# Performance work log

Measured on AMD Instinct MI355X. Metric: run time of the kernel, lower is better.

Reference implementation:

```python
import math
import jax, jax.numpy as jnp
import numpy as np

B, T, D = 2, 2048, 1024
NH = 16
HD = D // NH


def setup_inputs() -> dict:
    key = jax.random.key(0)
    k1, k2, k3 = jax.random.split(key, 3)
    s = 0.02
    return {
        "x": jax.random.normal(k1, (B, T, D), dtype=jnp.float32),
        "w_qkv": jax.random.normal(k2, (D, 3 * D), dtype=jnp.float32) * s,
        "w_proj": jax.random.normal(k3, (D, D), dtype=jnp.float32) * s,
    }


def reference(x, w_qkv, w_proj):
    b, t, c = x.shape
    qkv = x @ w_qkv  # [B,T,3D]
    q, k, v = jnp.split(qkv, 3, axis=-1)
    # [B,NH,T,HD]
    q = q.reshape(b, t, NH, HD).transpose(0, 2, 1, 3)
    k = k.reshape(b, t, NH, HD).transpose(0, 2, 1, 3)
    v = v.reshape(b, t, NH, HD).transpose(0, 2, 1, 3)
    scores = jnp.einsum("bhqd,bhkd->bhqk", q, k) / math.sqrt(HD)
    mask = jnp.tril(jnp.ones((t, t), dtype=x.dtype))  # [T,T]
    # faithful to source: scaled scores are multiplied by the mask, then -1e9 added where masked
    masked = scores * mask + (1.0 - mask) * (-1e9)
    a = jax.nn.softmax(masked, axis=-1)
    out = jnp.einsum("bhqk,bhkd->bhqd", a, v)  # [B,NH,T,HD]
    out = out.transpose(0, 2, 1, 3).reshape(b, t, c)
    return out @ w_proj
```

## Files before the change

kernel.cpp:

```cpp
#include <hip/hip_runtime.h>
#include <stdint.h>

#define B_SZ 2
#define T_SEQ 2048
#define D_MODEL 1024
#define NHEADS 16
#define HDIM 64
#define QKV_P (3 * D_MODEL)

typedef unsigned short u16;
typedef uint32_t u32;
typedef __attribute__((ext_vector_type(4))) float f32x4;
typedef __attribute__((ext_vector_type(8))) short s16x8;
typedef __attribute__((ext_vector_type(4))) short s16x4;

__device__ __forceinline__ u16 f2bf(float f) {
  union { float f; uint32_t u; } v; v.f = f;
  uint32_t r = v.u + 0x7fffu + ((v.u >> 16) & 1u);
  return (u16)(r >> 16);
}

__device__ __forceinline__ float fastexp2(float x) {
  float r;
  asm volatile("v_exp_f32 %0, %1" : "=v"(r) : "v"(x));
  return r;
}

__device__ __forceinline__ u32 cvtpk(float lo, float hi) {
  u32 r;
  asm volatile("v_cvt_pk_bf16_f32 %0, %1, %2" : "=v"(r) : "v"(lo), "v"(hi));
  return r;
}

__device__ __forceinline__ void async16(const void* g, void* l) {
  __builtin_amdgcn_global_load_lds((const __attribute__((address_space(1))) void*)g,
                                   (__attribute__((address_space(3))) void*)l,
                                   16, 0, 0);
}

__device__ __forceinline__ void rawbar() {
  __builtin_amdgcn_s_barrier();
  __builtin_amdgcn_sched_barrier(0);
}

__global__ __launch_bounds__(256) void prep(const float* __restrict__ x,
                                            const float* __restrict__ wq,
                                            const float* __restrict__ wp,
                                            u16* __restrict__ xb,
                                            u16* __restrict__ wqkvT,
                                            u16* __restrict__ wprojT) {
  const int bid = blockIdx.x, tid = threadIdx.x;
  if (bid < 4096) {
    int i = bid * 256 + tid;
    float4 v = ((const float4*)x)[i];
    ushort4 o;
    o.x = f2bf(v.x); o.y = f2bf(v.y); o.z = f2bf(v.z); o.w = f2bf(v.w);
    ((ushort4*)xb)[i] = o;
    return;
  }
  __shared__ float tile[32][33];
  const float* in; u16* outp; int C, bx, by;
  if (bid < 4096 + 3072) {
    int bb = bid - 4096; in = wq; outp = wqkvT; C = 3072; bx = bb % 96; by = bb / 96;
  } else {
    int bb = bid - 7168; in = wp; outp = wprojT; C = 1024; bx = bb % 32; by = bb / 32;
  }
  const int tx = tid & 31, ty = tid >> 5;
  const int c0 = bx * 32, r0 = by * 32;
#pragma unroll
  for (int i = 0; i < 4; i++)
    tile[ty + i * 8][tx] = in[(size_t)(r0 + ty + i * 8) * C + c0 + tx];
  __syncthreads();
#pragma unroll
  for (int i = 0; i < 4; i++)
    outp[(size_t)(c0 + ty + i * 8) * D_MODEL + r0 + tx] = f2bf(tile[tx][ty + i * 8]);
}

template <int F32OUT, int VFUSE, int NBN>
__global__ __launch_bounds__(256, 4) void gemm128k32(const u16* __restrict__ A,
                                                     const u16* __restrict__ BT,
                                                     void* __restrict__ Cout,
                                                     u16* __restrict__ vTout,
                                                     int N) {
  __shared__ u16 As[2][128 * 32];
  __shared__ u16 Bs[2][128 * 32];
  const int tid = threadIdx.x;
  const int lane = tid & 63, w = tid >> 6;
  const int l15 = lane & 15, g = lane >> 4;
  const int wr = w >> 1, wc = w & 1;
  const int id = blockIdx.x;
  const int cid = id >> 3;
  const int bm = (id & 7) * 4 + cid / NBN;
  const int bn = cid % NBN;
  const int K = 1024;
  const u16* Ab = A + (size_t)bm * 128 * K;
  const u16* Bb = BT + (size_t)bn * 128 * K;
  f32x4 acc[4][4];
#pragma unroll
  for (int i = 0; i < 4; i++)
#pragma unroll
    for (int j = 0; j < 4; j++) acc[i][j] = (f32x4){0.f, 0.f, 0.f, 0.f};

#define LD32(dst, srcb, kt_)                                                 \
  do {                                                                       \
    _Pragma("unroll") for (int i_ = 0; i_ < 2; i_++) {                       \
      int o_ = (tid + i_ * 256) * 16;                                        \
      int lo_ = o_ ^ (((o_ >> 6) & 3) << 4);                                 \
      async16((srcb) + (size_t)(lo_ >> 6) * K + (kt_) + ((lo_ & 63) >> 1),   \
              (char*)(dst) + o_);                                            \
    }                                                                        \
  } while (0)

  LD32(As[0], Ab, 0);
  LD32(Bs[0], Bb, 0);
  int cur = 0;
  for (int t = 0; t < 32; t++) {
    if (t < 31) {
      LD32(As[cur ^ 1], Ab, (t + 1) * 32);
      LD32(Bs[cur ^ 1], Bb, (t + 1) * 32);
      asm volatile("s_waitcnt vmcnt(4)" ::: "memory");
    } else {
      asm volatile("s_waitcnt vmcnt(0)" ::: "memory");
    }
    rawbar();
    s16x8 af[4], bf[4];
#pragma unroll
    for (int i = 0; i < 4; i++) {
      int r_ = wr * 64 + i * 16 + l15;
      af[i] = *(const s16x8*)((const char*)As[cur] +
                              ((r_ * 64 + g * 16) ^ ((r_ & 3) << 4)));
    }
#pragma unroll
    for (int jn = 0; jn < 4; jn++) {
      int n_ = wc * 64 + jn * 16 + l15;
      bf[jn] = *(const s16x8*)((const char*)Bs[cur] +
                               ((n_ * 64 + g * 16) ^ ((n_ & 3) << 4)));
    }
    __builtin_amdgcn_s_setprio(1);
#pragma unroll
    for (int i = 0; i < 4; i++)
#pragma unroll
      for (int jn = 0; jn < 4; jn++)
        acc[i][jn] = __builtin_amdgcn_mfma_f32_16x16x32_bf16(af[i], bf[jn], acc[i][jn], 0, 0, 0);
    __builtin_amdgcn_s_setprio(0);
    rawbar();
    cur ^= 1;
  }

  if (VFUSE && bn >= 16) {
#pragma unroll
    for (int i = 0; i < 4; i++) {
      const int m = bm * 128 + wr * 64 + i * 16 + g * 4;
      const int bloc = m >> 11;
      const int tl = m & 2047;
#pragma unroll
      for (int jn = 0; jn < 4; jn++) {
        const int hh = bn * 128 + wc * 64 + jn * 16 + l15 - 2048;
        uint2 pk;
        pk.x = cvtpk(acc[i][jn][0], acc[i][jn][1]);
        pk.y = cvtpk(acc[i][jn][2], acc[i][jn][3]);
        *(uint2*)&vTout[(size_t)(bloc * 1024 + hh) * T_SEQ + tl] = pk;
      }
    }
    return;
  }
#pragma unroll
  for (int i = 0; i < 4; i++) {
    const int row0 = bm * 128 + wr * 64 + i * 16 + g * 4;
#pragma unroll
    for (int jn = 0; jn < 4; jn++) {
      const int col = bn * 128 + wc * 64 + jn * 16 + l15;
#pragma unroll
      for (int r = 0; r < 4; r++) {
        if (F32OUT)
          ((float*)Cout)[(size_t)(row0 + r) * N + col] = acc[i][jn][r];
        else
          ((u16*)Cout)[(size_t)(row0 + r) * N + col] = f2bf(acc[i][jn][r]);
      }
    }
  }
}

template <int F32OUT, int VFUSE, int NBN>
__global__ __launch_bounds__(256, 2) void gemm128(const u16* __restrict__ A,
                                                  const u16* __restrict__ BT,
                                                  void* __restrict__ Cout,
                                                  u16* __restrict__ vTout,
                                                  int N) {
  __shared__ u16 As[2][128 * 64];
  __shared__ u16 Bs[2][128 * 64];
  const int tid = threadIdx.x;
  const int lane = tid & 63, w = tid >> 6;
  const int l15 = lane & 15, g = lane >> 4;
  const int wr = w >> 1, wc = w & 1;
  const int id = blockIdx.x;
  const int cid = id >> 3;
  const int bm = (id & 7) * 4 + cid / NBN;
  const int bn = cid % NBN;
  const int K = 1024;
  const u16* Ab = A + (size_t)bm * 128 * K;
  const u16* Bb = BT + (size_t)bn * 128 * K;
  f32x4 acc[4][4];
#pragma unroll
  for (int i = 0; i < 4; i++)
#pragma unroll
    for (int j = 0; j < 4; j++) acc[i][j] = (f32x4){0.f, 0.f, 0.f, 0.f};

#define G1_LD(dst, srcb, kt_)                                                \
  do {                                                                       \
    _Pragma("unroll") for (int i_ = 0; i_ < 4; i_++) {                       \
      int o_ = (tid + i_ * 256) * 16;                                        \
      int lo_ = o_ ^ (((o_ >> 7) & 7) << 4);                                 \
      async16((srcb) + (size_t)(lo_ >> 7) * K + (kt_) + ((lo_ & 127) >> 1),  \
              (char*)(dst) + o_);                                            \
    }                                                                        \
  } while (0)

  G1_LD(As[0], Ab, 0);
  G1_LD(Bs[0], Bb, 0);
  int cur = 0;
  for (int t = 0; t < 16; t++) {
    if (t < 15) {
      G1_LD(As[cur ^ 1], Ab, (t + 1) * 64);
      G1_LD(Bs[cur ^ 1], Bb, (t + 1) * 64);
      asm volatile("s_waitcnt vmcnt(8)" ::: "memory");
    } else {
      asm volatile("s_waitcnt vmcnt(0)" ::: "memory");
    }
    rawbar();
    s16x8 af[4][2], bf[4][2];
#pragma unroll
    for (int i = 0; i < 4; i++) {
      int r_ = wr * 64 + i * 16 + l15;
#pragma unroll
      for (int kk = 0; kk < 2; kk++)
        af[i][kk] = *(const s16x8*)((const char*)As[cur] +
                                    ((r_ * 128 + kk * 64 + g * 16) ^ ((r_ & 7) << 4)));
    }
#pragma unroll
    for (int jn = 0; jn < 4; jn++) {
      int n_ = wc * 64 + jn * 16 + l15;
#pragma unroll
      for (int kk = 0; kk < 2; kk++)
        bf[jn][kk] = *(const s16x8*)((const char*)Bs[cur] +
                                     ((n_ * 128 + kk * 64 + g * 16) ^ ((n_ & 7) << 4)));
    }
    __builtin_amdgcn_s_setprio(1);
#pragma unroll
    for (int i = 0; i < 4; i++)
#pragma unroll
      for (int jn = 0; jn < 4; jn++) {
        acc[i][jn] = __builtin_amdgcn_mfma_f32_16x16x32_bf16(af[i][0], bf[jn][0], acc[i][jn], 0, 0, 0);
        acc[i][jn] = __builtin_amdgcn_mfma_f32_16x16x32_bf16(af[i][1], bf[jn][1], acc[i][jn], 0, 0, 0);
      }
    __builtin_amdgcn_s_setprio(0);
    rawbar();
    cur ^= 1;
  }

  if (VFUSE && bn >= 16) {
#pragma unroll
    for (int i = 0; i < 4; i++) {
      const int m = bm * 128 + wr * 64 + i * 16 + g * 4;
      const int bloc = m >> 11;
      const int tl = m & 2047;
#pragma unroll
      for (int jn = 0; jn < 4; jn++) {
        const int hh = bn * 128 + wc * 64 + jn * 16 + l15 - 2048;
        uint2 pk;
        pk.x = cvtpk(acc[i][jn][0], acc[i][jn][1]);
        pk.y = cvtpk(acc[i][jn][2], acc[i][jn][3]);
        *(uint2*)&vTout[(size_t)(bloc * 1024 + hh) * T_SEQ + tl] = pk;
      }
    }
    return;
  }
#pragma unroll
  for (int i = 0; i < 4; i++) {
    const int row0 = bm * 128 + wr * 64 + i * 16 + g * 4;
#pragma unroll
    for (int jn = 0; jn < 4; jn++) {
      const int col = bn * 128 + wc * 64 + jn * 16 + l15;
#pragma unroll
      for (int r = 0; r < 4; r++) {
        if (F32OUT)
          ((float*)Cout)[(size_t)(row0 + r) * N + col] = acc[i][jn][r];
        else
          ((u16*)Cout)[(size_t)(row0 + r) * N + col] = f2bf(acc[i][jn][r]);
      }
    }
  }
}

__global__ __launch_bounds__(256, 4) void flash_attn(const u16* __restrict__ qkv,
                                                     const u16* __restrict__ vT,
                                                     u16* __restrict__ attn) {
  __shared__ u16 Ks[2][64 * 64];
  __shared__ u16 Vs[2][64 * 64];
  const int tid = threadIdx.x;
  const int lane = tid & 63, w = tid >> 6;
  const int l15 = lane & 15, g = lane >> 4;
  const int id = blockIdx.x;
  const int bh = ((id & 7) << 2) | ((id >> 3) & 3);
  const int j = (id >> 5) & 7, k4 = (id >> 8) & 3;
  const int qs = (k4 == 0) ? (31 - j) : (k4 == 1) ? (16 + j) : (k4 == 2) ? (15 - j) : j;
  const int b = bh >> 4, h = bh & 15;

  const size_t qrow = (size_t)(b * T_SEQ + qs * 64 + w * 16 + l15);
  s16x8 qf[2];
  qf[0] = *(const s16x8*)(qkv + qrow * QKV_P + h * HDIM + 0 * 32 + g * 8);
  qf[1] = *(const s16x8*)(qkv + qrow * QKV_P + h * HDIM + 1 * 32 + g * 8);

  f32x4 O[4];
#pragma unroll
  for (int t = 0; t < 4; t++) O[t] = (f32x4){0.f, 0.f, 0.f, 0.f};
  f32x4 sumacc = (f32x4){0.f, 0.f, 0.f, 0.f};
  float m_s = -1e30f;
  const int qrl = w * 16 + l15;
  const float sc = 0.18033688011112042f;
  const s16x4 onesf = {(short)0x3F80, (short)0x3F80, (short)0x3F80, (short)0x3F80};

#define STAGE(buf, kvt_)                                                                     \
  do {                                                                                       \
    _Pragma("unroll") for (int i_ = 0; i_ < 2; i_++) {                                       \
      int o_ = (tid + i_ * 256) * 16;                                                        \
      int lo_ = o_ ^ (((o_ >> 7) & 7) << 4);                                                 \
      int row_ = lo_ >> 7;                                                                   \
      int byt_ = lo_ & 127;                                                                  \
      async16(qkv + (size_t)(b * T_SEQ + (kvt_) * 64 + row_) * QKV_P + D_MODEL + h * HDIM +  \
                  (byt_ >> 1),                                                               \
              (char*)Ks[buf] + o_);                                                          \
      async16(vT + (size_t)(bh * HDIM + row_) * T_SEQ + (kvt_) * 64 + (byt_ >> 1),           \
              (char*)Vs[buf] + o_);                                                          \
    }                                                                                        \
  } while (0)

  STAGE(0, 0);
  int cur = 0;
  const int nt = qs + 1;
  for (int kvt = 0; kvt < nt; ++kvt) {
    if (kvt < qs) {
      STAGE(cur ^ 1, kvt + 1);
      asm volatile("s_waitcnt vmcnt(4)" ::: "memory");
    } else {
      asm volatile("s_waitcnt vmcnt(0)" ::: "memory");
    }
    rawbar();

    f32x4 S[4];
#pragma unroll
    for (int t16 = 0; t16 < 4; t16++) S[t16] = (f32x4){0.f, 0.f, 0.f, 0.f};
#pragma unroll
    for (int t16 = 0; t16 < 4; t16++)
#pragma unroll
      for (int kk = 0; kk < 2; kk++) {
        int key = t16 * 16 + l15;
        int bp = (key * 128 + kk * 64 + g * 16) ^ ((key & 7) << 4);
        s16x8 kf = *(const s16x8*)((const char*)Ks[cur] + bp);
        S[t16] = __builtin_amdgcn_mfma_f32_16x16x32_bf16(kf, qf[kk], S[t16], 0, 0, 0);
      }

    if (kvt == qs) {
#pragma unroll
      for (int t16 = 0; t16 < 4; t16++)
#pragma unroll
        for (int r = 0; r < 4; r++)
          if (t16 * 16 + g * 4 + r > qrl) S[t16][r] = -3e38f;
    }
    float pmx = fmaxf(fmaxf(fmaxf(S[0][0], S[0][1]), fmaxf(S[0][2], S[0][3])),
                      fmaxf(fmaxf(S[1][0], S[1][1]), fmaxf(S[1][2], S[1][3])));
    pmx = fmaxf(pmx, fmaxf(fmaxf(fmaxf(S[2][0], S[2][1]), fmaxf(S[2][2], S[2][3])),
                           fmaxf(fmaxf(S[3][0], S[3][1]), fmaxf(S[3][2], S[3][3]))));
    if (!__all(pmx - m_s <= 40.f)) {
      float mx = fmaxf(pmx, __shfl_xor(pmx, 16));
      mx = fmaxf(mx, __shfl_xor(mx, 32));
      const float mnew = fmaxf(m_s, mx);
      const float alpha = fastexp2((m_s - mnew) * sc);
      m_s = mnew;
      sumacc[0] *= alpha; sumacc[1] *= alpha; sumacc[2] *= alpha; sumacc[3] *= alpha;
#pragma unroll
      for (int t = 0; t < 4; t++)
#pragma unroll
        for (int r = 0; r < 4; r++) O[t][r] *= alpha;
    }
    const float msc = m_s * sc;
    float p[16];
#pragma unroll
    for (int t16 = 0; t16 < 4; t16++)
#pragma unroll
      for (int r = 0; r < 4; r++) p[t16 * 4 + r] = fastexp2(fmaf(S[t16][r], sc, -msc));

#pragma unroll
    for (int t16 = 0; t16 < 4; t16++) {
      union { u32 u[2]; s16x4 v; } pbv;
      pbv.u[0] = cvtpk(p[t16 * 4 + 0], p[t16 * 4 + 1]);
      pbv.u[1] = cvtpk(p[t16 * 4 + 2], p[t16 * 4 + 3]);
      sumacc = __builtin_amdgcn_mfma_f32_16x16x16bf16_1k(onesf, pbv.v, sumacc, 0, 0, 0);
#pragma unroll
      for (int t = 0; t < 4; t++) {
        int hd = t * 16 + l15;
        int bp = (hd * 128 + t16 * 32 + g * 8) ^ ((hd & 7) << 4);
        s16x4 vf = *(const s16x4*)((const char*)Vs[cur] + bp);
        O[t] = __builtin_amdgcn_mfma_f32_16x16x16bf16_1k(vf, pbv.v, O[t], 0, 0, 0);
      }
    }
    rawbar();
    cur ^= 1;
  }

  const float inv = 1.0f / sumacc[0];
  const size_t row = (size_t)(b * T_SEQ + qs * 64 + w * 16 + l15);
#pragma unroll
  for (int t = 0; t < 4; t++)
#pragma unroll
    for (int pr = 0; pr < 2; pr++) {
      u32 pk = cvtpk(O[t][pr * 2 + 0] * inv, O[t][pr * 2 + 1] * inv);
      *(u32*)&attn[row * D_MODEL + h * HDIM + t * 16 + g * 4 + pr * 2] = pk;
    }
}

extern "C" void kernel_launch(void* const* d_in, const int* in_sizes, int n_in,
                              void* d_out, int out_size, void* d_ws, size_t ws_size,
                              hipStream_t stream) {
  const float* x = (const float*)d_in[0];
  const float* w_qkv = (const float*)d_in[1];
  const float* w_proj = (const float*)d_in[2];
  float* out = (float*)d_out;
  char* ws = (char*)d_ws;
  const size_t MB = (size_t)1 << 20;
  if (ws_size < 56 * MB) return;
  u16* xb = (u16*)(ws + 0);
  u16* wqkvT = (u16*)(ws + 8 * MB);
  u16* wprojT = (u16*)(ws + 14 * MB);
  u16* qkv = (u16*)(ws + 16 * MB);
  u16* vT = (u16*)(ws + 40 * MB);
  u16* attn = (u16*)(ws + 48 * MB);

  prep<<<8192, 256, 0, stream>>>(x, w_qkv, w_proj, xb, wqkvT, wprojT);
  gemm128k32<0, 1, 24><<<768, 256, 0, stream>>>(xb, wqkvT, qkv, vT, QKV_P);
  flash_attn<<<1024, 256, 0, stream>>>(qkv, vT, attn);
  gemm128<1, 0, 8><<<256, 256, 0, stream>>>(attn, wprojT, out, nullptr, D_MODEL);
}
```

Before: 102.7 us.

## Software-pipeline attention loop: overlap QK of next tile with softmax/PV of previous

Restructures the flash-attention inner loop so the QK^T MFMAs for KV tile i are issued alongside the softmax and PV work for tile i-1, with the score tile carried across iterations. K and V staging are split so a single vmcnt(2) wait covers the newest K tile and the previous V tile, and the next tile's loads are issued after the barrier. The causal mask and final softmax/PV step are peeled out of the loop. The aim is to keep MFMA and exp/VALU work interleaved and hide load latency, at the cost of holding more live registers, which could hurt occupancy.

```diff
diff --git a/kernel.cpp b/kernel.cpp
--- a/kernel.cpp
+++ b/kernel.cpp
@@ -320,93 +320,99 @@
   const float sc = 0.18033688011112042f;
   const s16x4 onesf = {(short)0x3F80, (short)0x3F80, (short)0x3F80, (short)0x3F80};
 
-#define STAGE(buf, kvt_)                                                                     \
+#define STAGEK(buf, kvt_)                                                                    \
   do {                                                                                       \
     _Pragma("unroll") for (int i_ = 0; i_ < 2; i_++) {                                       \
       int o_ = (tid + i_ * 256) * 16;                                                        \
       int lo_ = o_ ^ (((o_ >> 7) & 7) << 4);                                                 \
-      int row_ = lo_ >> 7;                                                                   \
-      int byt_ = lo_ & 127;                                                                  \
-      async16(qkv + (size_t)(b * T_SEQ + (kvt_) * 64 + row_) * QKV_P + D_MODEL + h * HDIM +  \
-                  (byt_ >> 1),                                                               \
+      async16(qkv + (size_t)(b * T_SEQ + (kvt_) * 64 + (lo_ >> 7)) * QKV_P + D_MODEL +       \
+                  h * HDIM + ((lo_ & 127) >> 1),                                             \
               (char*)Ks[buf] + o_);                                                          \
-      async16(vT + (size_t)(bh * HDIM + row_) * T_SEQ + (kvt_) * 64 + (byt_ >> 1),           \
+    }                                                                                        \
+  } while (0)
+#define STAGEV(buf, kvt_)                                                                    \
+  do {                                                                                       \
+    _Pragma("unroll") for (int i_ = 0; i_ < 2; i_++) {                                       \
+      int o_ = (tid + i_ * 256) * 16;                                                        \
+      int lo_ = o_ ^ (((o_ >> 7) & 7) << 4);                                                 \
+      async16(vT + (size_t)(bh * HDIM + (lo_ >> 7)) * T_SEQ + (kvt_) * 64 +                  \
+                  ((lo_ & 127) >> 1),                                                        \
               (char*)Vs[buf] + o_);                                                          \
     }                                                                                        \
   } while (0)
 
-  STAGE(0, 0);
-  int cur = 0;
+#define SOFTMAX_PV(Sx, vb_)                                                                  \
+  {                                                                                          \
+    float pmx_ = fmaxf(fmaxf(fmaxf(Sx[0][0], Sx[0][1]), fmaxf(Sx[0][2], Sx[0][3])),          \
+                       fmaxf(fmaxf(Sx[1][0], Sx[1][1]), fmaxf(Sx[1][2], Sx[1][3])));         \
+    pmx_ = fmaxf(pmx_, fmaxf(fmaxf(fmaxf(Sx[2][0], Sx[2][1]), fmaxf(Sx[2][2], Sx[2][3])),    \
+                             fmaxf(fmaxf(Sx[3][0], Sx[3][1]), fmaxf(Sx[3][2], Sx[3][3]))));  \
+    if (!__all(pmx_ - m_s <= 40.f)) {                                                        \
+      float mx_ = fmaxf(pmx_, __shfl_xor(pmx_, 16));                                         \
+      mx_ = fmaxf(mx_, __shfl_xor(mx_, 32));                                                 \
+      const float mnew_ = fmaxf(m_s, mx_);                                                   \
+      const float alpha_ = fastexp2((m_s - mnew_) * sc);                                     \
+      m_s = mnew_;                                                                           \
+      sumacc[0] *= alpha_; sumacc[1] *= alpha_; sumacc[2] *= alpha_; sumacc[3] *= alpha_;    \
+      _Pragma("unroll") for (int t = 0; t < 4; t++)                                          \
+      _Pragma("unroll") for (int r = 0; r < 4; r++) O[t][r] *= alpha_;                       \
+    }                                                                                        \
+    const float msc_ = m_s * sc;                                                             \
+    float p_[16];                                                                            \
+    _Pragma("unroll") for (int t16 = 0; t16 < 4; t16++)                                      \
+    _Pragma("unroll") for (int r = 0; r < 4; r++)                                            \
+        p_[t16 * 4 + r] = fastexp2(fmaf(Sx[t16][r], sc, -msc_));                             \
+    _Pragma("unroll") for (int t16 = 0; t16 < 4; t16++) {                                    \
+      union { u32 u[2]; s16x4 v; } pbv_;                                                     \
+      pbv_.u[0] = cvtpk(p_[t16 * 4 + 0], p_[t16 * 4 + 1]);                                   \
+      pbv_.u[1] = cvtpk(p_[t16 * 4 + 2], p_[t16 * 4 + 3]);                                   \
+      sumacc = __builtin_amdgcn_mfma_f32_16x16x16bf16_1k(onesf, pbv_.v, sumacc, 0, 0, 0);    \
+      _Pragma("unroll") for (int t = 0; t < 4; t++) {                                        \
+        int hd_ = t * 16 + l15;                                                              \
+        int bp_ = (hd_ * 128 + t16 * 32 + g * 8) ^ ((hd_ & 7) << 4);                         \
+        s16x4 vf_ = *(const s16x4*)((const char*)Vs[vb_] + bp_);                             \
+        O[t] = __builtin_amdgcn_mfma_f32_16x16x16bf16_1k(vf_, pbv_.v, O[t], 0, 0, 0);        \
+      }                                                                                      \
+    }                                                                                        \
+  }
+
+  STAGEK(0, 0);
+  STAGEV(0, 0);
+  f32x4 Sp[4];
   const int nt = qs + 1;
-  for (int kvt = 0; kvt < nt; ++kvt) {
-    if (kvt < qs) {
-      STAGE(cur ^ 1, kvt + 1);
-      asm volatile("s_waitcnt vmcnt(4)" ::: "memory");
-    } else {
-      asm volatile("s_waitcnt vmcnt(0)" ::: "memory");
-    }
-    rawbar();
-
-    f32x4 S[4];
-#pragma unroll
-    for (int t16 = 0; t16 < 4; t16++) S[t16] = (f32x4){0.f, 0.f, 0.f, 0.f};
+  for (int i = 0; i < nt; ++i) {
+    asm volatile("s_waitcnt vmcnt(2)" ::: "memory");
+    rawbar();
+    f32x4 Sn[4];
+#pragma unroll
+    for (int t16 = 0; t16 < 4; t16++) Sn[t16] = (f32x4){0.f, 0.f, 0.f, 0.f};
 #pragma unroll
     for (int t16 = 0; t16 < 4; t16++)
 #pragma unroll
       for (int kk = 0; kk < 2; kk++) {
         int key = t16 * 16 + l15;
         int bp = (key * 128 + kk * 64 + g * 16) ^ ((key & 7) << 4);
-        s16x8 kf = *(const s16x8*)((const char*)Ks[cur] + bp);
-        S[t16] = __builtin_amdgcn_mfma_f32_16x16x32_bf16(kf, qf[kk], S[t16], 0, 0, 0);
-      }
-
-    if (kvt == qs) {
-#pragma unroll
-      for (int t16 = 0; t16 < 4; t16++)
-#pragma unroll
-        for (int r = 0; r < 4; r++)
-          if (t16 * 16 + g * 4 + r > qrl) S[t16][r] = -3e38f;
-    }
-    float pmx = fmaxf(fmaxf(fmaxf(S[0][0], S[0][1]), fmaxf(S[0][2], S[0][3])),
-                      fmaxf(fmaxf(S[1][0], S[1][1]), fmaxf(S[1][2], S[1][3])));
-    pmx = fmaxf(pmx, fmaxf(fmaxf(fmaxf(S[2][0], S[2][1]), fmaxf(S[2][2], S[2][3])),
-                           fmaxf(fmaxf(S[3][0], S[3][1]), fmaxf(S[3][2], S[3][3]))));
-    if (!__all(pmx - m_s <= 40.f)) {
-      float mx = fmaxf(pmx, __shfl_xor(pmx, 16));
-      mx = fmaxf(mx, __shfl_xor(mx, 32));
-      const float mnew = fmaxf(m_s, mx);
-      const float alpha = fastexp2((m_s - mnew) * sc);
-      m_s = mnew;
-      sumacc[0] *= alpha; sumacc[1] *= alpha; sumacc[2] *= alpha; sumacc[3] *= alpha;
-#pragma unroll
-      for (int t = 0; t < 4; t++)
-#pragma unroll
-        for (int r = 0; r < 4; r++) O[t][r] *= alpha;
-    }
-    const float msc = m_s * sc;
-    float p[16];
-#pragma unroll
-    for (int t16 = 0; t16 < 4; t16++)
-#pragma unroll
-      for (int r = 0; r < 4; r++) p[t16 * 4 + r] = fastexp2(fmaf(S[t16][r], sc, -msc));
-
-#pragma unroll
-    for (int t16 = 0; t16 < 4; t16++) {
-      union { u32 u[2]; s16x4 v; } pbv;
-      pbv.u[0] = cvtpk(p[t16 * 4 + 0], p[t16 * 4 + 1]);
-      pbv.u[1] = cvtpk(p[t16 * 4 + 2], p[t16 * 4 + 3]);
-      sumacc = __builtin_amdgcn_mfma_f32_16x16x16bf16_1k(onesf, pbv.v, sumacc, 0, 0, 0);
-#pragma unroll
-      for (int t = 0; t < 4; t++) {
-        int hd = t * 16 + l15;
-        int bp = (hd * 128 + t16 * 32 + g * 8) ^ ((hd & 7) << 4);
-        s16x4 vf = *(const s16x4*)((const char*)Vs[cur] + bp);
-        O[t] = __builtin_amdgcn_mfma_f32_16x16x16bf16_1k(vf, pbv.v, O[t], 0, 0, 0);
-      }
-    }
-    rawbar();
-    cur ^= 1;
-  }
+        s16x8 kf = *(const s16x8*)((const char*)Ks[i & 1] + bp);
+        Sn[t16] = __builtin_amdgcn_mfma_f32_16x16x32_bf16(kf, qf[kk], Sn[t16], 0, 0, 0);
+      }
+    if (i > 0) {
+      SOFTMAX_PV(Sp, (i - 1) & 1);
+    }
+    rawbar();
+    if (i + 1 < nt) {
+      STAGEK((i + 1) & 1, i + 1);
+      STAGEV((i + 1) & 1, i + 1);
+    }
+    Sp[0] = Sn[0]; Sp[1] = Sn[1]; Sp[2] = Sn[2]; Sp[3] = Sn[3];
+  }
+  asm volatile("s_waitcnt vmcnt(0)" ::: "memory");
+  rawbar();
+#pragma unroll
+  for (int t16 = 0; t16 < 4; t16++)
+#pragma unroll
+    for (int r = 0; r < 4; r++)
+      if (t16 * 16 + g * 4 + r > qrl) Sp[t16][r] = -3e38f;
+  SOFTMAX_PV(Sp, (nt - 1) & 1);
 
   const float inv = 1.0f / sumacc[0];
   const size_t row = (size_t)(b * T_SEQ + qs * 64 + w * 16 + l15);
```

Result: no change. 102.4 us (-0.3%).

## Give each wave private K/V staging buffers and drop block barriers in attention

Applied to the files above, without the earlier changes.

Each of the four waves now stages its own copy of the K and V tiles into private LDS regions, processing 32-key chunks instead of shared 64-key tiles. This removes both workgroup barriers per iteration, since every wave only waits on its own async loads. In exchange, each K/V tile is fetched four times from global/L2, LDS use grows to 64KB per block with launch bounds lowered to 2, and the loop runs twice as many shorter iterations.

```diff
diff --git a/kernel.cpp b/kernel.cpp
--- a/kernel.cpp
+++ b/kernel.cpp
@@ -292,11 +292,10 @@
   }
 }
 
-__global__ __launch_bounds__(256, 4) void flash_attn(const u16* __restrict__ qkv,
+__global__ __launch_bounds__(256, 2) void flash_attn(const u16* __restrict__ qkv,
                                                      const u16* __restrict__ vT,
                                                      u16* __restrict__ attn) {
-  __shared__ u16 Ks[2][64 * 64];
-  __shared__ u16 Vs[2][64 * 64];
+  __shared__ u16 lds[4][8192];
   const int tid = threadIdx.x;
   const int lane = tid & 63, w = tid >> 6;
   const int l15 = lane & 15, g = lane >> 4;
@@ -320,57 +319,53 @@
   const float sc = 0.18033688011112042f;
   const s16x4 onesf = {(short)0x3F80, (short)0x3F80, (short)0x3F80, (short)0x3F80};
 
-#define STAGE(buf, kvt_)                                                                     \
+#define STAGE32(buf_, kvt_)                                                                  \
   do {                                                                                       \
-    _Pragma("unroll") for (int i_ = 0; i_ < 2; i_++) {                                       \
-      int o_ = (tid + i_ * 256) * 16;                                                        \
+    _Pragma("unroll") for (int i_ = 0; i_ < 4; i_++) {                                       \
+      int o_ = (lane + i_ * 64) * 16;                                                        \
       int lo_ = o_ ^ (((o_ >> 7) & 7) << 4);                                                 \
-      int row_ = lo_ >> 7;                                                                   \
-      int byt_ = lo_ & 127;                                                                  \
-      async16(qkv + (size_t)(b * T_SEQ + (kvt_) * 64 + row_) * QKV_P + D_MODEL + h * HDIM +  \
-                  (byt_ >> 1),                                                               \
-              (char*)Ks[buf] + o_);                                                          \
-      async16(vT + (size_t)(bh * HDIM + row_) * T_SEQ + (kvt_) * 64 + (byt_ >> 1),           \
-              (char*)Vs[buf] + o_);                                                          \
+      async16(qkv + (size_t)(b * T_SEQ + (kvt_) * 32 + (lo_ >> 7)) * QKV_P + D_MODEL +       \
+                  h * HDIM + ((lo_ & 127) >> 1),                                             \
+              (char*)&lds[w][(buf_)*2048] + o_);                                             \
+      int vo_ = o_ ^ (((o_ >> 6) & 3) << 4);                                                 \
+      async16(vT + (size_t)(bh * HDIM + (vo_ >> 6)) * T_SEQ + (kvt_) * 32 +                  \
+                  ((vo_ & 63) >> 1),                                                         \
+              (char*)&lds[w][4096 + (buf_)*2048] + o_);                                      \
     }                                                                                        \
   } while (0)
 
-  STAGE(0, 0);
+  STAGE32(0, 0);
   int cur = 0;
-  const int nt = qs + 1;
-  for (int kvt = 0; kvt < nt; ++kvt) {
-    if (kvt < qs) {
-      STAGE(cur ^ 1, kvt + 1);
-      asm volatile("s_waitcnt vmcnt(4)" ::: "memory");
+  const int nt = 2 * qs + 2;
+  for (int i = 0; i < nt; ++i) {
+    if (i + 1 < nt) {
+      STAGE32(cur ^ 1, i + 1);
+      asm volatile("s_waitcnt vmcnt(8)" ::: "memory");
     } else {
       asm volatile("s_waitcnt vmcnt(0)" ::: "memory");
     }
-    rawbar();
-
-    f32x4 S[4];
-#pragma unroll
-    for (int t16 = 0; t16 < 4; t16++) S[t16] = (f32x4){0.f, 0.f, 0.f, 0.f};
-#pragma unroll
-    for (int t16 = 0; t16 < 4; t16++)
+    f32x4 S[2];
+#pragma unroll
+    for (int t16 = 0; t16 < 2; t16++) S[t16] = (f32x4){0.f, 0.f, 0.f, 0.f};
+#pragma unroll
+    for (int t16 = 0; t16 < 2; t16++)
 #pragma unroll
       for (int kk = 0; kk < 2; kk++) {
         int key = t16 * 16 + l15;
         int bp = (key * 128 + kk * 64 + g * 16) ^ ((key & 7) << 4);
-        s16x8 kf = *(const s16x8*)((const char*)Ks[cur] + bp);
+        s16x8 kf = *(const s16x8*)((const char*)&lds[w][cur * 2048] + bp);
         S[t16] = __builtin_amdgcn_mfma_f32_16x16x32_bf16(kf, qf[kk], S[t16], 0, 0, 0);
       }
-
-    if (kvt == qs) {
-#pragma unroll
-      for (int t16 = 0; t16 < 4; t16++)
+    if (i >= nt - 2) {
+      const int kb = i * 32 - qs * 64;
+#pragma unroll
+      for (int t16 = 0; t16 < 2; t16++)
 #pragma unroll
         for (int r = 0; r < 4; r++)
-          if (t16 * 16 + g * 4 + r > qrl) S[t16][r] = -3e38f;
+          if (kb + t16 * 16 + g * 4 + r > qrl) S[t16][r] = -3e38f;
     }
     float pmx = fmaxf(fmaxf(fmaxf(S[0][0], S[0][1]), fmaxf(S[0][2], S[0][3])),
                       fmaxf(fmaxf(S[1][0], S[1][1]), fmaxf(S[1][2], S[1][3])));
-    pmx = fmaxf(pmx, fmaxf(fmaxf(fmaxf(S[2][0], S[2][1]), fmaxf(S[2][2], S[2][3])),
-                           fmaxf(fmaxf(S[3][0], S[3][1]), fmaxf(S[3][2], S[3][3]))));
     if (!__all(pmx - m_s <= 40.f)) {
       float mx = fmaxf(pmx, __shfl_xor(pmx, 16));
       mx = fmaxf(mx, __shfl_xor(mx, 32));
@@ -384,14 +379,13 @@
         for (int r = 0; r < 4; r++) O[t][r] *= alpha;
     }
     const float msc = m_s * sc;
-    float p[16];
-#pragma unroll
-    for (int t16 = 0; t16 < 4; t16++)
+    float p[8];
+#pragma unroll
+    for (int t16 = 0; t16 < 2; t16++)
 #pragma unroll
       for (int r = 0; r < 4; r++) p[t16 * 4 + r] = fastexp2(fmaf(S[t16][r], sc, -msc));
-
-#pragma unroll
-    for (int t16 = 0; t16 < 4; t16++) {
+#pragma unroll
+    for (int t16 = 0; t16 < 2; t16++) {
       union { u32 u[2]; s16x4 v; } pbv;
       pbv.u[0] = cvtpk(p[t16 * 4 + 0], p[t16 * 4 + 1]);
       pbv.u[1] = cvtpk(p[t16 * 4 + 2], p[t16 * 4 + 3]);
@@ -399,12 +393,11 @@
 #pragma unroll
       for (int t = 0; t < 4; t++) {
         int hd = t * 16 + l15;
-        int bp = (hd * 128 + t16 * 32 + g * 8) ^ ((hd & 7) << 4);
-        s16x4 vf = *(const s16x4*)((const char*)Vs[cur] + bp);
+        int bp = (hd * 64 + t16 * 32 + g * 8) ^ ((hd & 3) << 4);
+        s16x4 vf = *(const s16x4*)((const char*)&lds[w][4096 + cur * 2048] + bp);
         O[t] = __builtin_amdgcn_mfma_f32_16x16x16bf16_1k(vf, pbv.v, O[t], 0, 0, 0);
       }
     }
-    rawbar();
     cur ^= 1;
   }
 
```

Result: slower. 116.0 us (+12.9%).

## Triple-buffer GEMM shared-memory stages to prefetch two K-tiles ahead

Applied to the files above, without the earlier changes.

Replaces the double-buffered A/B shared-memory tiles in the bf16 GEMM with a three-stage ring buffer. Loads are now issued two K-steps ahead, and the vmcnt waits are adjusted so more global-load latency overlaps with MFMA work. Shared memory per block grows from 32KB to 48KB, so launch bounds drop from 4 to 3 blocks per CU, which may reduce occupancy.

```diff
diff --git a/kernel.cpp b/kernel.cpp
--- a/kernel.cpp
+++ b/kernel.cpp
@@ -77,13 +77,12 @@
 }
 
 template <int F32OUT, int VFUSE, int NBN>
-__global__ __launch_bounds__(256, 4) void gemm128k32(const u16* __restrict__ A,
+__global__ __launch_bounds__(256, 3) void gemm128k32(const u16* __restrict__ A,
                                                      const u16* __restrict__ BT,
                                                      void* __restrict__ Cout,
                                                      u16* __restrict__ vTout,
                                                      int N) {
-  __shared__ u16 As[2][128 * 32];
-  __shared__ u16 Bs[2][128 * 32];
+  __shared__ u16 SS[3][8192];
   const int tid = threadIdx.x;
   const int lane = tid & 63, w = tid >> 6;
   const int l15 = lane & 15, g = lane >> 4;
@@ -101,7 +100,7 @@
 #pragma unroll
     for (int j = 0; j < 4; j++) acc[i][j] = (f32x4){0.f, 0.f, 0.f, 0.f};
 
-#define LD32(dst, srcb, kt_)                                                 \
+#define LD32B(dst, srcb, kt_)                                                \
   do {                                                                       \
     _Pragma("unroll") for (int i_ = 0; i_ < 2; i_++) {                       \
       int o_ = (tid + i_ * 256) * 16;                                        \
@@ -110,31 +109,37 @@
               (char*)(dst) + o_);                                            \
     }                                                                        \
   } while (0)
-
-  LD32(As[0], Ab, 0);
-  LD32(Bs[0], Bb, 0);
-  int cur = 0;
+#define STG(bi_, kt_)                        \
+  do {                                       \
+    LD32B((char*)SS[bi_], Ab, kt_);          \
+    LD32B((char*)SS[bi_] + 8192, Bb, kt_);   \
+  } while (0)
+
+  STG(0, 0);
+  STG(1, 32);
+  int cur = 0, nxt = 2;
   for (int t = 0; t < 32; t++) {
-    if (t < 31) {
-      LD32(As[cur ^ 1], Ab, (t + 1) * 32);
-      LD32(Bs[cur ^ 1], Bb, (t + 1) * 32);
+    if (t < 30) {
+      STG(nxt, (t + 2) * 32);
+      asm volatile("s_waitcnt vmcnt(8)" ::: "memory");
+    } else if (t == 30) {
       asm volatile("s_waitcnt vmcnt(4)" ::: "memory");
     } else {
       asm volatile("s_waitcnt vmcnt(0)" ::: "memory");
     }
     rawbar();
+    const char* Abase = (const char*)SS[cur];
+    const char* Bbase = Abase + 8192;
     s16x8 af[4], bf[4];
 #pragma unroll
     for (int i = 0; i < 4; i++) {
       int r_ = wr * 64 + i * 16 + l15;
-      af[i] = *(const s16x8*)((const char*)As[cur] +
-                              ((r_ * 64 + g * 16) ^ ((r_ & 3) << 4)));
+      af[i] = *(const s16x8*)(Abase + ((r_ * 64 + g * 16) ^ ((r_ & 3) << 4)));
     }
 #pragma unroll
     for (int jn = 0; jn < 4; jn++) {
       int n_ = wc * 64 + jn * 16 + l15;
-      bf[jn] = *(const s16x8*)((const char*)Bs[cur] +
-                               ((n_ * 64 + g * 16) ^ ((n_ & 3) << 4)));
+      bf[jn] = *(const s16x8*)(Bbase + ((n_ * 64 + g * 16) ^ ((n_ & 3) << 4)));
     }
     __builtin_amdgcn_s_setprio(1);
 #pragma unroll
@@ -144,7 +149,8 @@
         acc[i][jn] = __builtin_amdgcn_mfma_f32_16x16x32_bf16(af[i], bf[jn], acc[i][jn], 0, 0, 0);
     __builtin_amdgcn_s_setprio(0);
     rawbar();
-    cur ^= 1;
+    cur = (cur == 2) ? 0 : cur + 1;
+    nxt = (nxt == 2) ? 0 : nxt + 1;
   }
 
   if (VFUSE && bn >= 16) {
```

Result: no change. 103.6 us (+0.9%).
